# Kernel tuning notes

Hardware: AMD Instinct MI355X
Metric: run time of the kernel (lower is better)

Reference implementation:

```python
import jax, jax.numpy as jnp
import numpy as np

N_NODES = 50000
N_EDGES = 800000
NUM_EMBS = 50000
EMB = 128
HID = 256
OUT = 128
NUM_GRAPHS = 256


def gcn_conv(x, W, b, src, dst, n):
    # PyG GCNConv: add self-loops, sym-normalize, aggregate, linear.
    h = x @ W  # [n, d_out]
    ones = jnp.ones((src.shape[0],), dtype=x.dtype)
    deg = jax.ops.segment_sum(ones, dst, num_segments=n) + 1.0  # +1 self-loop
    dinv = jax.lax.rsqrt(deg)  # deg^{-1/2}
    norm = dinv[src] * dinv[dst]  # per-edge norm
    msg = h[src] * norm[:, None]  # gather + scale  [E, d_out]
    agg = jax.ops.segment_sum(msg, dst, num_segments=n)
    agg = agg + h * (dinv * dinv)[:, None]  # self-loop term 1/deg[i]
    return agg + b


def scatter_mean(x, seg, num_segments):
    s = jax.ops.segment_sum(x, seg, num_segments=num_segments)
    cnt = jax.ops.segment_sum(jnp.ones((x.shape[0],), x.dtype), seg, num_segments=num_segments)
    return s / jnp.maximum(cnt, 1.0)[:, None]


def setup_inputs() -> dict:
    key = jax.random.key(0)
    ks = jax.random.split(key, 12)
    node_ids = jax.random.randint(ks[0], (N_NODES,), 0, NUM_EMBS)
    edge_index = jax.random.randint(ks[1], (2, N_EDGES), 0, N_NODES)
    batch = jnp.sort(jax.random.randint(ks[2], (N_NODES,), 0, NUM_GRAPHS))
    s = 0.05
    embed = jax.random.normal(ks[3], (NUM_EMBS, EMB), jnp.float32) * s
    W_in = jax.random.normal(ks[4], (EMB, HID), jnp.float32) * s
    b_in = jnp.zeros((HID,), jnp.float32)
    W_h1 = jax.random.normal(ks[5], (HID, HID), jnp.float32) * s
    b_h1 = jnp.zeros((HID,), jnp.float32)
    W_h2 = jax.random.normal(ks[6], (HID, HID), jnp.float32) * s
    b_h2 = jnp.zeros((HID,), jnp.float32)
    W_out = jax.random.normal(ks[7], (HID, OUT), jnp.float32) * s
    b_out = jnp.zeros((OUT,), jnp.float32)
    return {"node_ids": node_ids, "edge_index": edge_index, "batch": batch,
            "embed": embed, "W_in": W_in, "b_in": b_in,
            "W_h1": W_h1, "b_h1": b_h1, "W_h2": W_h2, "b_h2": b_h2,
            "W_out": W_out, "b_out": b_out}


def reference(node_ids, edge_index, batch, embed, W_in, b_in, W_h1, b_h1, W_h2, b_h2, W_out, b_out):
    src, dst = edge_index[0], edge_index[1]
    n = node_ids.shape[0]
    x = embed[node_ids]  # [N, EMB]
    x = gcn_conv(x, W_in, b_in, src, dst, n)
    x = jax.nn.relu(x)  # dropout = identity (eval mode)
    for W, b in ((W_h1, b_h1), (W_h2, b_h2)):
        x = gcn_conv(x, W, b, src, dst, n) + x  # residual
        x = jax.nn.relu(x)
    x = gcn_conv(x, W_out, b_out, src, dst, n)
    return scatter_mean(x, batch, NUM_GRAPHS)  # [NUM_GRAPHS, OUT]
```

## Files before the change

kernel.cpp:

```cpp
#include <hip/hip_runtime.h>
#include <hip/hip_bf16.h>
#include <hip/hip_fp8.h>

#define N_NODES 50000
#define N_EDGES 800000
#define EMB_D 128
#define HID_D 256
#define OUT_D 128
#define NGRAPH 256

#define SCAN_B ((N_NODES + 256) / 256)
#define MAX_CSR (N_EDGES + 7 * N_NODES)

typedef __attribute__((ext_vector_type(8))) short short8;
typedef __attribute__((ext_vector_type(4))) float floatx4;
typedef __attribute__((ext_vector_type(4))) unsigned short ushortx4;
typedef __attribute__((ext_vector_type(8))) unsigned short ushortx8;
typedef __attribute__((ext_vector_type(4))) unsigned char ucharx4;
typedef __attribute__((ext_vector_type(8))) unsigned char ucharx8;

__device__ inline unsigned short f2b(float f) {
    __hip_bfloat16 h = __float2bfloat16(f);
    return *reinterpret_cast<unsigned short*>(&h);
}

__device__ inline float b2f(unsigned short u) {
    union { unsigned int i; float f; } c;
    c.i = ((unsigned int)u) << 16;
    return c.f;
}

__device__ inline unsigned char f2f8(float f) {
    __hip_fp8_e4m3 v(f);
    return (unsigned char)v.__x;
}

__device__ inline float h2f(unsigned short u) { return b2f(u); }
__device__ inline float h2f(unsigned char u) {
    __hip_fp8_e4m3 v; v.__x = (__hip_fp8_storage_t)u;
    return (float)v;
}

template<int D, typename HT> struct HVec;
template<> struct HVec<128, unsigned short> { using T = ushortx4; };
template<> struct HVec<256, unsigned short> { using T = ushortx8; };
template<> struct HVec<128, unsigned char>  { using T = ucharx4;  };
template<> struct HVec<256, unsigned char>  { using T = ucharx8;  };

__global__ void rank_kernel(const int* __restrict__ dst, int* __restrict__ deg4,
                            int* __restrict__ pos) {
    int e = blockIdx.x * blockDim.x + threadIdx.x;
    if (e >= N_EDGES) return;
    pos[e] = atomicAdd(&deg4[(size_t)(e & 3) * N_NODES + dst[e]], 1);
}

__global__ void scan_a(const int* __restrict__ deg4, int* __restrict__ degt,
                       int* __restrict__ degp, int* __restrict__ sb4,
                       int* __restrict__ bsum, float* __restrict__ dinv) {
    __shared__ int red[256];
    int t = threadIdx.x;
    int i = blockIdx.x * 256 + t;
    int pad = 0;
    if (i < N_NODES) {
        int d0 = deg4[i];
        int d1 = deg4[(size_t)N_NODES + i];
        int d2 = deg4[(size_t)2 * N_NODES + i];
        int d3 = deg4[(size_t)3 * N_NODES + i];
        int tot = d0 + d1 + d2 + d3;
        degt[i] = tot;
        pad = (tot + 7) & ~7;
        degp[i] = pad;
        dinv[i] = rsqrtf((float)tot + 1.0f);
        sb4[i] = 0;
        sb4[(size_t)N_NODES + i] = d0;
        sb4[(size_t)2 * N_NODES + i] = d0 + d1;
        sb4[(size_t)3 * N_NODES + i] = d0 + d1 + d2;
    }
    red[t] = pad;
    __syncthreads();
    for (int off = 128; off > 0; off >>= 1) {
        if (t < off) red[t] += red[t + off];
        __syncthreads();
    }
    if (t == 0) bsum[blockIdx.x] = red[0];
}

__global__ void scan_b(const int* __restrict__ bsum, int* __restrict__ boff,
                       const int* __restrict__ batch, int* __restrict__ bstart) {
    int t = threadIdx.x;
    {
        int lo = 0, hi = N_NODES;
        while (lo < hi) {
            int mid = (lo + hi) >> 1;
            if (batch[mid] < t) lo = mid + 1;
            else hi = mid;
        }
        bstart[t] = lo;
        if (t == 0) bstart[NGRAPH] = N_NODES;
    }
    __shared__ int s[256];
    s[t] = (t < SCAN_B) ? bsum[t] : 0;
    __syncthreads();
    for (int off = 1; off < 256; off <<= 1) {
        int v = (t >= off) ? s[t - off] : 0;
        __syncthreads();
        s[t] += v;
        __syncthreads();
    }
    if (t < SCAN_B) boff[t] = (t == 0) ? 0 : s[t - 1];
}

__global__ void scan_c(const int* __restrict__ degp, const int* __restrict__ degt,
                       const int* __restrict__ boff, int* __restrict__ row_start,
                       int2* __restrict__ csr_sn) {
    __shared__ int s[256];
    int t = threadIdx.x;
    int i = blockIdx.x * 256 + t;
    int v = (i < N_NODES) ? degp[i] : 0;
    s[t] = v;
    __syncthreads();
    for (int off = 1; off < 256; off <<= 1) {
        int x = (t >= off) ? s[t - off] : 0;
        __syncthreads();
        s[t] += x;
        __syncthreads();
    }
    int excl = s[t] - v;
    int rs = boff[blockIdx.x] + excl;
    if (i <= N_NODES) row_start[i] = rs;
    if (i < N_NODES) {
        int e_true = rs + degt[i];
        int e_end  = rs + degp[i];
        for (int k = e_true; k < e_end; ++k) csr_sn[k] = make_int2(0, 0);
    }
}

__global__ void scatter_kernel(const int* __restrict__ src, const int* __restrict__ dst,
                               const int* __restrict__ pos, const int* __restrict__ row_start,
                               const int* __restrict__ sb4, const float* __restrict__ dinv,
                               int2* __restrict__ csr_sn) {
    int e = blockIdx.x * blockDim.x + threadIdx.x;
    if (e >= N_EDGES) return;
    int s = src[e], d = dst[e];
    int slot = row_start[d] + sb4[(size_t)(e & 3) * N_NODES + d] + pos[e];
    csr_sn[slot] = make_int2(s, __float_as_int(dinv[s] * dinv[d]));
}

__global__ void gather_bf16(const int* __restrict__ ids, const float* __restrict__ embed,
                            unsigned short* __restrict__ X0) {
    int idx = blockIdx.x * blockDim.x + threadIdx.x;
    const int V = EMB_D / 4;
    if (idx >= N_NODES * V) return;
    int row = idx / V, c = idx % V;
    float4 v = ((const float4*)embed)[(size_t)ids[row] * V + c];
    ushortx4 u;
    u[0] = f2b(v.x); u[1] = f2b(v.y); u[2] = f2b(v.z); u[3] = f2b(v.w);
    ((ushortx4*)X0)[idx] = u;
}

template<int D, typename HT, bool HASB, bool RES, bool RELU, bool BOUT>
__global__ __launch_bounds__(256) void agg_node(
        const int* __restrict__ row_start, const int2* __restrict__ csr_sn,
        const float* __restrict__ dinv, const HT* __restrict__ H,
        const float* __restrict__ b, float* __restrict__ OUTF,
        unsigned short* __restrict__ Pb) {
    constexpr int V2 = D / 32;
    using UV = typename HVec<D, HT>::T;
    using RV = typename HVec<D, unsigned short>::T;
    int wave = threadIdx.x >> 6, lane = threadIdx.x & 63;
    int i = blockIdx.x * 4 + wave;
    if (i >= N_NODES) return;
    int h = lane >> 5, q = lane & 31;
    const int off = q * V2;
    const HT* __restrict__ Hoff = H + off;
    float acc0[V2], acc1[V2];
#pragma unroll
    for (int v = 0; v < V2; ++v) { acc0[v] = 0.f; acc1[v] = 0.f; }
    int e0 = row_start[i], e1 = row_start[i + 1];
    if (e0 < e1) {
        int2 sn0 = csr_sn[e0 + h];
        int2 sn1 = csr_sn[e0 + 2 + h];
        int2 sn2 = csr_sn[e0 + 4 + h];
        int2 sn3 = csr_sn[e0 + 6 + h];
        int e = e0 + 8;
        for (;;) {
            UV u0 = *(const UV*)(Hoff + (size_t)sn0.x * D);
            UV u1 = *(const UV*)(Hoff + (size_t)sn1.x * D);
            UV u2 = *(const UV*)(Hoff + (size_t)sn2.x * D);
            UV u3 = *(const UV*)(Hoff + (size_t)sn3.x * D);
            float n0 = __int_as_float(sn0.y), n1 = __int_as_float(sn1.y);
            float n2 = __int_as_float(sn2.y), n3 = __int_as_float(sn3.y);
            bool more = (e < e1);
            int2 t0, t1, t2, t3;
            if (more) {
                t0 = csr_sn[e + h];
                t1 = csr_sn[e + 2 + h];
                t2 = csr_sn[e + 4 + h];
                t3 = csr_sn[e + 6 + h];
            }
#pragma unroll
            for (int v = 0; v < V2; ++v) acc0[v] = fmaf(h2f(u0[v]), n0, acc0[v]);
#pragma unroll
            for (int v = 0; v < V2; ++v) acc1[v] = fmaf(h2f(u1[v]), n1, acc1[v]);
#pragma unroll
            for (int v = 0; v < V2; ++v) acc0[v] = fmaf(h2f(u2[v]), n2, acc0[v]);
#pragma unroll
            for (int v = 0; v < V2; ++v) acc1[v] = fmaf(h2f(u3[v]), n3, acc1[v]);
            if (!more) break;
            sn0 = t0; sn1 = t1; sn2 = t2; sn3 = t3;
            e += 8;
        }
    }
#pragma unroll
    for (int v = 0; v < V2; ++v) {
        float s = acc0[v] + acc1[v];
        acc0[v] = s + __shfl_xor(s, 32);
    }
    if (h == 0) {
        float di = dinv[i];
        float d2 = di * di;
        UV us = *(const UV*)(Hoff + (size_t)i * D);
        RV rb;
        if (RES) rb = *(const RV*)(Pb + (size_t)i * D + off);
        RV ob;
#pragma unroll
        for (int v = 0; v < V2; ++v) {
            float val = acc0[v];
            val = fmaf(h2f(us[v]), d2, val);
            if (HASB) val += b[off + v];
            if (RES)  val += b2f(rb[v]);
            if (RELU) val = fmaxf(val, 0.f);
            if (BOUT) ob[v] = f2b(val);
            else      OUTF[(size_t)i * D + off + v] = val;
        }
        if (BOUT) *(RV*)(Pb + (size_t)i * D + off) = ob;
    }
}

template<int K, int D>
__device__ inline void wsplit_one(int idx, const float* __restrict__ W,
                                  short* __restrict__ wb) {
    int j = idx & 7;
    int l = (idx >> 3) & 63;
    int rest = idx >> 9;
    int kb = rest % (K / 32);
    int t = rest / (K / 32);
    int k = kb * 32 + (l >> 4) * 8 + j;
    int ncol = t * 16 + (l & 15);
    wb[idx] = (short)f2b(W[(size_t)k * D + ncol]);
}

__global__ void wsplit_all(const float* __restrict__ W_in, const float* __restrict__ W_h1,
                           const float* __restrict__ W_h2, const float* __restrict__ W_out,
                           short* __restrict__ wb_in, short* __restrict__ wb_h1,
                           short* __restrict__ wb_h2, short* __restrict__ wb_out) {
    int idx = blockIdx.x * blockDim.x + threadIdx.x;
    constexpr int S1 = EMB_D * HID_D;
    constexpr int S2 = S1 + HID_D * HID_D;
    constexpr int S3 = S2 + HID_D * HID_D;
    constexpr int S4 = S3 + HID_D * OUT_D;
    if (idx < S1)      wsplit_one<EMB_D, HID_D>(idx,      W_in,  wb_in);
    else if (idx < S2) wsplit_one<HID_D, HID_D>(idx - S1, W_h1,  wb_h1);
    else if (idx < S3) wsplit_one<HID_D, HID_D>(idx - S2, W_h2,  wb_h2);
    else if (idx < S4) wsplit_one<HID_D, OUT_D>(idx - S3, W_out, wb_out);
}

template<int K, int D, bool BIAS, bool RELU, int OMODE>
__global__ __launch_bounds__(256) void gemm_mfma(
        const unsigned short* __restrict__ A_g, const short* __restrict__ Wb,
        const float* __restrict__ b, void* __restrict__ OutB, int n) {
    constexpr int LDK = K + 8;
    constexpr int NT = D / 64;
    constexpr int KB = K / 32;
    __shared__ __align__(16) short Ab[64 * LDK];

    int row0 = blockIdx.x * 64;
    constexpr int NF8 = 64 * (K / 8);
    for (int idx = threadIdx.x; idx < NF8; idx += 256) {
        int r = idx / (K / 8), c8 = idx % (K / 8);
        ushortx8 vh = {0, 0, 0, 0, 0, 0, 0, 0};
        if (row0 + r < n)
            vh = *(const ushortx8*)(A_g + (size_t)(row0 + r) * K + c8 * 8);
        *(ushortx8*)&Ab[r * LDK + c8 * 8] = vh;
    }
    __syncthreads();

    int wave = threadIdx.x >> 6, lane = threadIdx.x & 63;
    int quad = lane >> 4, lane15 = lane & 15;

    floatx4 acc[4][NT];
#pragma unroll
    for (int mt = 0; mt < 4; ++mt)
#pragma unroll
        for (int nt = 0; nt < NT; ++nt)
            acc[mt][nt] = (floatx4){0.f, 0.f, 0.f, 0.f};

#pragma unroll
    for (int kb = 0; kb < KB; ++kb) {
        short8 ah[4];
#pragma unroll
        for (int mt = 0; mt < 4; ++mt) {
            int addr = (mt * 16 + lane15) * LDK + kb * 32 + quad * 8;
            ah[mt] = *(const short8*)&Ab[addr];
        }
        short8 bh[NT];
#pragma unroll
        for (int nt = 0; nt < NT; ++nt) {
            int t = wave * NT + nt;
            size_t fb = ((size_t)(t * KB + kb) * 64 + lane) * 8;
            bh[nt] = *(const short8*)&Wb[fb];
        }
#pragma unroll
        for (int mt = 0; mt < 4; ++mt)
#pragma unroll
            for (int nt = 0; nt < NT; ++nt)
                acc[mt][nt] = __builtin_amdgcn_mfma_f32_16x16x32_bf16(ah[mt], bh[nt], acc[mt][nt], 0, 0, 0);
    }

#pragma unroll
    for (int mt = 0; mt < 4; ++mt) {
#pragma unroll
        for (int nt = 0; nt < NT; ++nt) {
            int col = wave * (NT * 16) + nt * 16 + lane15;
            float bj = BIAS ? b[col] : 0.f;
#pragma unroll
            for (int reg = 0; reg < 4; ++reg) {
                int row = row0 + mt * 16 + quad * 4 + reg;
                if (row < n) {
                    float v = acc[mt][nt][reg] + bj;
                    if (RELU) v = fmaxf(v, 0.f);
                    if (OMODE == 2) ((unsigned char*)OutB)[(size_t)row * D + col] = f2f8(v);
                    else            ((unsigned short*)OutB)[(size_t)row * D + col] = f2b(v);
                }
            }
        }
    }
}

__global__ void graph_mean(const int* __restrict__ bstart, const float* __restrict__ X,
                           float* __restrict__ out) {
    int g = blockIdx.x;
    int r0 = bstart[g], r1 = bstart[g + 1];
    int col = threadIdx.x & 127, rr = threadIdx.x >> 7;
    float acc = 0.f;
    for (int r = r0 + rr; r < r1; r += 2)
        acc += X[(size_t)r * OUT_D + col];
    __shared__ float sh[128];
    if (rr == 1) sh[col] = acc;
    __syncthreads();
    if (rr == 0) {
        float tot = acc + sh[col];
        int c = r1 - r0;
        out[(size_t)g * OUT_D + col] = tot / (float)(c > 0 ? c : 1);
    }
}

extern "C" void kernel_launch(void* const* d_in, const int* in_sizes, int n_in,
                              void* d_out, int out_size, void* d_ws, size_t ws_size,
                              hipStream_t stream) {
    const int* node_ids = (const int*)d_in[0];
    const int* edge_index = (const int*)d_in[1];
    const int* batch = (const int*)d_in[2];
    const float* embed = (const float*)d_in[3];
    const float* W_in  = (const float*)d_in[4];
    const float* b_in  = (const float*)d_in[5];
    const float* W_h1  = (const float*)d_in[6];
    const float* b_h1  = (const float*)d_in[7];
    const float* W_h2  = (const float*)d_in[8];
    const float* b_h2  = (const float*)d_in[9];
    const float* W_out = (const float*)d_in[10];
    const float* b_out = (const float*)d_in[11];
    float* out = (float*)d_out;

    const int* src = edge_index;
    const int* dst = edge_index + N_EDGES;

    char* w = (char*)d_ws;
    size_t o = 0;
    auto alloc = [&](size_t bytes) -> void* {
        void* p = w + o;
        o = (o + bytes + 255) & ~(size_t)255;
        return p;
    };
    int*   deg4     = (int*)alloc((size_t)4 * N_NODES * sizeof(int));
    int*   sb4      = (int*)alloc((size_t)4 * N_NODES * sizeof(int));
    int*   degt     = (int*)alloc((size_t)N_NODES * sizeof(int));
    int*   degp     = (int*)alloc((size_t)N_NODES * sizeof(int));
    int*   pos      = (int*)alloc((size_t)N_EDGES * sizeof(int));
    float* dinv     = (float*)alloc((size_t)N_NODES * sizeof(float));
    int*   bstart   = (int*)alloc((size_t)(NGRAPH + 1) * sizeof(int));
    int*   row_start= (int*)alloc((size_t)(N_NODES + 1) * sizeof(int));
    int*   bsum     = (int*)alloc((size_t)SCAN_B * sizeof(int));
    int*   boff     = (int*)alloc((size_t)SCAN_B * sizeof(int));
    int2*  csr_sn   = (int2*)alloc((size_t)MAX_CSR * sizeof(int2));
    unsigned short* Xb  = (unsigned short*)alloc((size_t)N_NODES * HID_D * sizeof(short));
    unsigned short* E16 = (unsigned short*)alloc((size_t)N_NODES * EMB_D * sizeof(short));
    unsigned char*  H8  = (unsigned char*)alloc((size_t)N_NODES * HID_D);
    unsigned short* A1b = (unsigned short*)alloc((size_t)N_NODES * 128 * sizeof(short));
    float* A1       = (float*)alloc((size_t)N_NODES * 128 * sizeof(float));
    short* Wb_in    = (short*)alloc((size_t)EMB_D * HID_D * sizeof(short));
    short* Wb_h1    = (short*)alloc((size_t)HID_D * HID_D * sizeof(short));
    short* Wb_h2    = (short*)alloc((size_t)HID_D * HID_D * sizeof(short));
    short* Wb_out   = (short*)alloc((size_t)HID_D * OUT_D * sizeof(short));
    unsigned char* H8_4 = H8;
    (void)ws_size;

    hipMemsetAsync(deg4, 0, (size_t)4 * N_NODES * sizeof(int), stream);

    rank_kernel<<<(N_EDGES + 255) / 256, 256, 0, stream>>>(dst, deg4, pos);
    scan_a<<<SCAN_B, 256, 0, stream>>>(deg4, degt, degp, sb4, bsum, dinv);
    scan_b<<<1, 256, 0, stream>>>(bsum, boff, batch, bstart);
    scan_c<<<SCAN_B, 256, 0, stream>>>(degp, degt, boff, row_start, csr_sn);
    scatter_kernel<<<(N_EDGES + 255) / 256, 256, 0, stream>>>(src, dst, pos, row_start,
                                                              sb4, dinv, csr_sn);

    wsplit_all<<<(196608 + 255) / 256, 256, 0, stream>>>(
        W_in, W_h1, W_h2, W_out, Wb_in, Wb_h1, Wb_h2, Wb_out);

    const int gemm_grid = (N_NODES + 63) / 64;
    const int agg_grid = (N_NODES + 3) / 4;

    gather_bf16<<<(N_NODES * (EMB_D / 4) + 255) / 256, 256, 0, stream>>>(node_ids, embed, E16);
    agg_node<128, unsigned short, false, false, false, true><<<agg_grid, 256, 0, stream>>>(
        row_start, csr_sn, dinv, E16, nullptr, nullptr, A1b);
    gemm_mfma<128, 256, true, true, 0><<<gemm_grid, 256, 0, stream>>>(
        A1b, Wb_in, b_in, Xb, N_NODES);

    gemm_mfma<256, 256, false, false, 2><<<gemm_grid, 256, 0, stream>>>(
        Xb, Wb_h1, nullptr, H8, N_NODES);
    agg_node<256, unsigned char, true, true, true, true><<<agg_grid, 256, 0, stream>>>(
        row_start, csr_sn, dinv, H8, b_h1, nullptr, Xb);

    gemm_mfma<256, 256, false, false, 2><<<gemm_grid, 256, 0, stream>>>(
        Xb, Wb_h2, nullptr, H8, N_NODES);
    agg_node<256, unsigned char, true, true, true, true><<<agg_grid, 256, 0, stream>>>(
        row_start, csr_sn, dinv, H8, b_h2, nullptr, Xb);

    gemm_mfma<256, 128, false, false, 2><<<gemm_grid, 256, 0, stream>>>(
        Xb, Wb_out, nullptr, H8_4, N_NODES);
    agg_node<128, unsigned char, true, false, false, false><<<agg_grid, 256, 0, stream>>>(
        row_start, csr_sn, dinv, H8_4, b_out, A1, nullptr);

    graph_mean<<<NGRAPH, 256, 0, stream>>>(bstart, A1, out);
}
```

Baseline: 424.7 us.

## Pack CSR into 32-bit entries, store embeddings as fp8, merge prep kernels

Each CSR entry becomes a single 32-bit word holding a 16-bit source index and a bf16 edge norm, which halves the index traffic in every aggregation pass. The gathered embedding table is now stored as fp8 rather than bf16, so the first aggregation reads half as many bytes. The embedding gather and the weight-splitting kernels are merged into one launch. The 16-bit index only works because N_NODES is below 65536, and the bf16 norm and fp8 embeddings lower precision.

```diff
diff --git a/kernel.cpp b/kernel.cpp
--- a/kernel.cpp
+++ b/kernel.cpp
@@ -112,7 +112,7 @@
 
 __global__ void scan_c(const int* __restrict__ degp, const int* __restrict__ degt,
                        const int* __restrict__ boff, int* __restrict__ row_start,
-                       int2* __restrict__ csr_sn) {
+                       unsigned int* __restrict__ csr) {
     __shared__ int s[256];
     int t = threadIdx.x;
     int i = blockIdx.x * 256 + t;
@@ -131,36 +131,65 @@
     if (i < N_NODES) {
         int e_true = rs + degt[i];
         int e_end  = rs + degp[i];
-        for (int k = e_true; k < e_end; ++k) csr_sn[k] = make_int2(0, 0);
+        for (int k = e_true; k < e_end; ++k) csr[k] = 0u;
     }
 }
 
 __global__ void scatter_kernel(const int* __restrict__ src, const int* __restrict__ dst,
                                const int* __restrict__ pos, const int* __restrict__ row_start,
                                const int* __restrict__ sb4, const float* __restrict__ dinv,
-                               int2* __restrict__ csr_sn) {
+                               unsigned int* __restrict__ csr) {
     int e = blockIdx.x * blockDim.x + threadIdx.x;
     if (e >= N_EDGES) return;
     int s = src[e], d = dst[e];
     int slot = row_start[d] + sb4[(size_t)(e & 3) * N_NODES + d] + pos[e];
-    csr_sn[slot] = make_int2(s, __float_as_int(dinv[s] * dinv[d]));
-}
-
-__global__ void gather_bf16(const int* __restrict__ ids, const float* __restrict__ embed,
-                            unsigned short* __restrict__ X0) {
+    csr[slot] = ((unsigned int)f2b(dinv[s] * dinv[d]) << 16) | (unsigned int)s;
+}
+
+template<int K, int D>
+__device__ inline void wsplit_one(int idx, const float* __restrict__ W,
+                                  short* __restrict__ wb) {
+    int j = idx & 7;
+    int l = (idx >> 3) & 63;
+    int rest = idx >> 9;
+    int kb = rest % (K / 32);
+    int t = rest / (K / 32);
+    int k = kb * 32 + (l >> 4) * 8 + j;
+    int ncol = t * 16 + (l & 15);
+    wb[idx] = (short)f2b(W[(size_t)k * D + ncol]);
+}
+
+__global__ void prep_kernel(const int* __restrict__ ids, const float* __restrict__ embed,
+                            unsigned char* __restrict__ E8,
+                            const float* __restrict__ W_in, const float* __restrict__ W_h1,
+                            const float* __restrict__ W_h2, const float* __restrict__ W_out,
+                            short* __restrict__ wb_in, short* __restrict__ wb_h1,
+                            short* __restrict__ wb_h2, short* __restrict__ wb_out) {
     int idx = blockIdx.x * blockDim.x + threadIdx.x;
-    const int V = EMB_D / 4;
-    if (idx >= N_NODES * V) return;
-    int row = idx / V, c = idx % V;
-    float4 v = ((const float4*)embed)[(size_t)ids[row] * V + c];
-    ushortx4 u;
-    u[0] = f2b(v.x); u[1] = f2b(v.y); u[2] = f2b(v.z); u[3] = f2b(v.w);
-    ((ushortx4*)X0)[idx] = u;
+    constexpr int GV = N_NODES * (EMB_D / 4);
+    if (idx < GV) {
+        const int V = EMB_D / 4;
+        int row = idx / V, c = idx % V;
+        float4 v = ((const float4*)embed)[(size_t)ids[row] * V + c];
+        ucharx4 u;
+        u[0] = f2f8(v.x); u[1] = f2f8(v.y); u[2] = f2f8(v.z); u[3] = f2f8(v.w);
+        ((ucharx4*)E8)[idx] = u;
+        return;
+    }
+    int j = idx - GV;
+    constexpr int S1 = EMB_D * HID_D;
+    constexpr int S2 = S1 + HID_D * HID_D;
+    constexpr int S3 = S2 + HID_D * HID_D;
+    constexpr int S4 = S3 + HID_D * OUT_D;
+    if (j < S1)      wsplit_one<EMB_D, HID_D>(j,      W_in,  wb_in);
+    else if (j < S2) wsplit_one<HID_D, HID_D>(j - S1, W_h1,  wb_h1);
+    else if (j < S3) wsplit_one<HID_D, HID_D>(j - S2, W_h2,  wb_h2);
+    else if (j < S4) wsplit_one<HID_D, OUT_D>(j - S3, W_out, wb_out);
 }
 
 template<int D, typename HT, bool HASB, bool RES, bool RELU, bool BOUT>
 __global__ __launch_bounds__(256) void agg_node(
-        const int* __restrict__ row_start, const int2* __restrict__ csr_sn,
+        const int* __restrict__ row_start, const unsigned int* __restrict__ csr,
         const float* __restrict__ dinv, const HT* __restrict__ H,
         const float* __restrict__ b, float* __restrict__ OUTF,
         unsigned short* __restrict__ Pb) {
@@ -178,25 +207,27 @@
     for (int v = 0; v < V2; ++v) { acc0[v] = 0.f; acc1[v] = 0.f; }
     int e0 = row_start[i], e1 = row_start[i + 1];
     if (e0 < e1) {
-        int2 sn0 = csr_sn[e0 + h];
-        int2 sn1 = csr_sn[e0 + 2 + h];
-        int2 sn2 = csr_sn[e0 + 4 + h];
-        int2 sn3 = csr_sn[e0 + 6 + h];
+        unsigned int sn0 = csr[e0 + h];
+        unsigned int sn1 = csr[e0 + 2 + h];
+        unsigned int sn2 = csr[e0 + 4 + h];
+        unsigned int sn3 = csr[e0 + 6 + h];
         int e = e0 + 8;
         for (;;) {
-            UV u0 = *(const UV*)(Hoff + (size_t)sn0.x * D);
-            UV u1 = *(const UV*)(Hoff + (size_t)sn1.x * D);
-            UV u2 = *(const UV*)(Hoff + (size_t)sn2.x * D);
-            UV u3 = *(const UV*)(Hoff + (size_t)sn3.x * D);
-            float n0 = __int_as_float(sn0.y), n1 = __int_as_float(sn1.y);
-            float n2 = __int_as_float(sn2.y), n3 = __int_as_float(sn3.y);
+            UV u0 = *(const UV*)(Hoff + (size_t)(sn0 & 0xFFFFu) * D);
+            UV u1 = *(const UV*)(Hoff + (size_t)(sn1 & 0xFFFFu) * D);
+            UV u2 = *(const UV*)(Hoff + (size_t)(sn2 & 0xFFFFu) * D);
+            UV u3 = *(const UV*)(Hoff + (size_t)(sn3 & 0xFFFFu) * D);
+            float n0 = b2f((unsigned short)(sn0 >> 16));
+            float n1 = b2f((unsigned short)(sn1 >> 16));
+            float n2 = b2f((unsigned short)(sn2 >> 16));
+            float n3 = b2f((unsigned short)(sn3 >> 16));
             bool more = (e < e1);
-            int2 t0, t1, t2, t3;
+            unsigned int t0, t1, t2, t3;
             if (more) {
-                t0 = csr_sn[e + h];
-                t1 = csr_sn[e + 2 + h];
-                t2 = csr_sn[e + 4 + h];
-                t3 = csr_sn[e + 6 + h];
+                t0 = csr[e + h];
+                t1 = csr[e + 2 + h];
+                t2 = csr[e + 4 + h];
+                t3 = csr[e + 6 + h];
             }
 #pragma unroll
             for (int v = 0; v < V2; ++v) acc0[v] = fmaf(h2f(u0[v]), n0, acc0[v]);
@@ -235,34 +266,6 @@
         }
         if (BOUT) *(RV*)(Pb + (size_t)i * D + off) = ob;
     }
-}
-
-template<int K, int D>
-__device__ inline void wsplit_one(int idx, const float* __restrict__ W,
-                                  short* __restrict__ wb) {
-    int j = idx & 7;
-    int l = (idx >> 3) & 63;
-    int rest = idx >> 9;
-    int kb = rest % (K / 32);
-    int t = rest / (K / 32);
-    int k = kb * 32 + (l >> 4) * 8 + j;
-    int ncol = t * 16 + (l & 15);
-    wb[idx] = (short)f2b(W[(size_t)k * D + ncol]);
-}
-
-__global__ void wsplit_all(const float* __restrict__ W_in, const float* __restrict__ W_h1,
-                           const float* __restrict__ W_h2, const float* __restrict__ W_out,
-                           short* __restrict__ wb_in, short* __restrict__ wb_h1,
-                           short* __restrict__ wb_h2, short* __restrict__ wb_out) {
-    int idx = blockIdx.x * blockDim.x + threadIdx.x;
-    constexpr int S1 = EMB_D * HID_D;
-    constexpr int S2 = S1 + HID_D * HID_D;
-    constexpr int S3 = S2 + HID_D * HID_D;
-    constexpr int S4 = S3 + HID_D * OUT_D;
-    if (idx < S1)      wsplit_one<EMB_D, HID_D>(idx,      W_in,  wb_in);
-    else if (idx < S2) wsplit_one<HID_D, HID_D>(idx - S1, W_h1,  wb_h1);
-    else if (idx < S3) wsplit_one<HID_D, HID_D>(idx - S2, W_h2,  wb_h2);
-    else if (idx < S4) wsplit_one<HID_D, OUT_D>(idx - S3, W_out, wb_out);
 }
 
 template<int K, int D, bool BIAS, bool RELU, int OMODE>
@@ -392,9 +395,9 @@
     int*   row_start= (int*)alloc((size_t)(N_NODES + 1) * sizeof(int));
     int*   bsum     = (int*)alloc((size_t)SCAN_B * sizeof(int));
     int*   boff     = (int*)alloc((size_t)SCAN_B * sizeof(int));
-    int2*  csr_sn   = (int2*)alloc((size_t)MAX_CSR * sizeof(int2));
+    unsigned int* csr = (unsigned int*)alloc((size_t)MAX_CSR * sizeof(unsigned int));
     unsigned short* Xb  = (unsigned short*)alloc((size_t)N_NODES * HID_D * sizeof(short));
-    unsigned short* E16 = (unsigned short*)alloc((size_t)N_NODES * EMB_D * sizeof(short));
+    unsigned char*  E8  = (unsigned char*)alloc((size_t)N_NODES * EMB_D);
     unsigned char*  H8  = (unsigned char*)alloc((size_t)N_NODES * HID_D);
     unsigned short* A1b = (unsigned short*)alloc((size_t)N_NODES * 128 * sizeof(short));
     float* A1       = (float*)alloc((size_t)N_NODES * 128 * sizeof(float));
@@ -410,36 +413,36 @@
     rank_kernel<<<(N_EDGES + 255) / 256, 256, 0, stream>>>(dst, deg4, pos);
     scan_a<<<SCAN_B, 256, 0, stream>>>(deg4, degt, degp, sb4, bsum, dinv);
     scan_b<<<1, 256, 0, stream>>>(bsum, boff, batch, bstart);
-    scan_c<<<SCAN_B, 256, 0, stream>>>(degp, degt, boff, row_start, csr_sn);
+    scan_c<<<SCAN_B, 256, 0, stream>>>(degp, degt, boff, row_start, csr);
     scatter_kernel<<<(N_EDGES + 255) / 256, 256, 0, stream>>>(src, dst, pos, row_start,
-                                                              sb4, dinv, csr_sn);
-
-    wsplit_all<<<(196608 + 255) / 256, 256, 0, stream>>>(
-        W_in, W_h1, W_h2, W_out, Wb_in, Wb_h1, Wb_h2, Wb_out);
+                                                              sb4, dinv, csr);
+
+    constexpr int GV = N_NODES * (EMB_D / 4);
+    prep_kernel<<<(GV + 196608 + 255) / 256, 256, 0, stream>>>(
+        node_ids, embed, E8, W_in, W_h1, W_h2, W_out, Wb_in, Wb_h1, Wb_h2, Wb_out);
 
     const int gemm_grid = (N_NODES + 63) / 64;
     const int agg_grid = (N_NODES + 3) / 4;
 
-    gather_bf16<<<(N_NODES * (EMB_D / 4) + 255) / 256, 256, 0, stream>>>(node_ids, embed, E16);
-    agg_node<128, unsigned short, false, false, false, true><<<agg_grid, 256, 0, stream>>>(
-        row_start, csr_sn, dinv, E16, nullptr, nullptr, A1b);
+    agg_node<128, unsigned char, false, false, false, true><<<agg_grid, 256, 0, stream>>>(
+        row_start, csr, dinv, E8, nullptr, nullptr, A1b);
     gemm_mfma<128, 256, true, true, 0><<<gemm_grid, 256, 0, stream>>>(
         A1b, Wb_in, b_in, Xb, N_NODES);
 
     gemm_mfma<256, 256, false, false, 2><<<gemm_grid, 256, 0, stream>>>(
         Xb, Wb_h1, nullptr, H8, N_NODES);
     agg_node<256, unsigned char, true, true, true, true><<<agg_grid, 256, 0, stream>>>(
-        row_start, csr_sn, dinv, H8, b_h1, nullptr, Xb);
+        row_start, csr, dinv, H8, b_h1, nullptr, Xb);
 
     gemm_mfma<256, 256, false, false, 2><<<gemm_grid, 256, 0, stream>>>(
         Xb, Wb_h2, nullptr, H8, N_NODES);
     agg_node<256, unsigned char, true, true, true, true><<<agg_grid, 256, 0, stream>>>(
-        row_start, csr_sn, dinv, H8, b_h2, nullptr, Xb);
+        row_start, csr, dinv, H8, b_h2, nullptr, Xb);
 
     gemm_mfma<256, 128, false, false, 2><<<gemm_grid, 256, 0, stream>>>(
         Xb, Wb_out, nullptr, H8_4, N_NODES);
     agg_node<128, unsigned char, true, false, false, false><<<agg_grid, 256, 0, stream>>>(
-        row_start, csr_sn, dinv, H8_4, b_out, A1, nullptr);
+        row_start, csr, dinv, H8_4, b_out, A1, nullptr);
 
     graph_mean<<<NGRAPH, 256, 0, stream>>>(bstart, A1, out);
 }
```

After: 395.7 us. 1.07x faster.
